# Performance work log

Measured on AMD Instinct MI355X. Metric: run time of the kernel, lower is better.

Reference implementation:

```python
import jax, jax.numpy as jnp
import numpy as np
from functools import partial

B, N, C = 16, 10647, 80   # batch, total anchors (YOLOv3@416), num classes
K = 2048                  # max candidates kept per image before NMS
SCORE_THR = 0.5
IOU_THR = 0.5


def setup_inputs() -> dict:
    key = jax.random.key(0)
    # [B, N, 4+1+C]: xywh (normalized), objectness, class probs
    y_pred = jax.random.uniform(key, (B, N, 5 + C), dtype=jnp.float32)
    return {"y_pred": y_pred}


def _xywh_to_corners(b):
    x, y, w, h = b[..., 0], b[..., 1], b[..., 2], b[..., 3]
    return jnp.stack([x - w / 2, y - h / 2, x + w / 2, y + h / 2], axis=-1)


def _pairwise_iou(boxes):  # boxes [K,4] corners -> [K,K]
    x1, y1, x2, y2 = boxes[:, 0], boxes[:, 1], boxes[:, 2], boxes[:, 3]
    area = jnp.maximum(x2 - x1, 0.0) * jnp.maximum(y2 - y1, 0.0)
    ix1 = jnp.maximum(x1[:, None], x1[None, :])
    iy1 = jnp.maximum(y1[:, None], y1[None, :])
    ix2 = jnp.minimum(x2[:, None], x2[None, :])
    iy2 = jnp.minimum(y2[:, None], y2[None, :])
    inter = jnp.maximum(ix2 - ix1, 0.0) * jnp.maximum(iy2 - iy1, 0.0)
    union = area[:, None] + area[None, :] - inter
    return inter / jnp.maximum(union, 1e-9)


def _greedy_nms_keep(boxes, valid):  # boxes [K,4] sorted by score desc, valid [K] bool
    iou = _pairwise_iou(boxes)
    idxs = jnp.arange(K)

    def body(i, keep):
        suppress = keep[i] & (idxs > i) & (iou[i] > IOU_THR)
        return keep & ~suppress

    return jax.lax.fori_loop(0, K, body, valid)


def reference(y_pred):
    boxes_xywh = y_pred[..., :4]           # [B,N,4]
    obj = y_pred[..., 4]                   # [B,N]
    cls_probs = y_pred[..., 5:]            # [B,N,C]
    scores = obj * jnp.max(cls_probs, axis=-1)  # [B,N]

    # top-K candidates per image (sorted by score desc)
    scores_k, idx = jax.lax.top_k(scores, K)             # [B,K]
    boxes_k = jnp.take_along_axis(boxes_xywh, idx[:, :, None], axis=1)  # [B,K,4]
    corners = _xywh_to_corners(boxes_k)                  # [B,K,4]

    valid = scores_k > SCORE_THR                          # [B,K]
    # NMS keep mask is a non-differentiable selection
    keep = jax.vmap(_greedy_nms_keep)(
        jax.lax.stop_gradient(corners), valid)            # [B,K] bool
    keep_f = keep.astype(scores_k.dtype)

    out_boxes = corners * keep_f[:, :, None]
    out_scores = scores_k * keep_f
    return jnp.concatenate([out_boxes, out_scores[:, :, None]], axis=-1)  # [B,K,5]
```

## Files before the change

kernel.cpp:

```cpp
#include <hip/hip_runtime.h>

#define BATCH 16
#define NROW  10647
#define ROWF  85
#define NCLS  80
#define KTOP  2048
#define MPAD  16384
#define SCORE_THR 0.5f
#define IOU_THR   0.5f

typedef unsigned long long u64;
typedef unsigned int u32;

__device__ __forceinline__ u32 enc_f32(float f) {
    u32 u = __float_as_uint(f);
    return (u & 0x80000000u) ? ~u : (u | 0x80000000u);
}
__device__ __forceinline__ float dec_f32(u32 e) {
    u32 u = (e & 0x80000000u) ? (e & 0x7FFFFFFFu) : ~e;
    return __uint_as_float(u);
}
__device__ __forceinline__ float bcast(float v, int ii) {
    return __uint_as_float(__builtin_amdgcn_readlane(__float_as_uint(v), ii));
}
__device__ __forceinline__ u64 rl64(u64 v, int l) {
    u32 lo = __builtin_amdgcn_readlane((u32)(v & 0xFFFFFFFFull), l);
    u32 hi = __builtin_amdgcn_readlane((u32)(v >> 32), l);
    return ((u64)hi << 32) | (u64)lo;
}
__device__ __forceinline__ void gload_lds16(const void* g, void* lds) {
    __builtin_amdgcn_global_load_lds(
        (const __attribute__((address_space(1))) void*)g,
        (__attribute__((address_space(3))) void*)lds, 16, 0, 0);
}
__device__ __forceinline__ void bar_lds() {
    asm volatile("s_waitcnt lgkmcnt(0)" ::: "memory");
    __builtin_amdgcn_s_barrier();
    __builtin_amdgcn_sched_barrier(0);
}

template<int J>
__device__ __forceinline__ void reg_pass(u64 v[8], int tid, int k) {
    #pragma unroll
    for (int r = 0; r < 8; ++r) {
        if (!(r & J)) {
            bool desc = (((tid * 8 + r) & k) == 0);
            u64 a = v[r], b = v[r | J];
            u64 mx = a > b ? a : b, mn = a > b ? b : a;
            v[r]     = desc ? mx : mn;
            v[r | J] = desc ? mn : mx;
        }
    }
}

__device__ __forceinline__ void shfl_pass(u64 v[8], int tid, int k, int d) {
    const bool upper = (tid & d) == 0;
    const bool desc = (((tid * 8) & k) == 0);
    const bool keepmax = (desc == upper);
    #pragma unroll
    for (int r = 0; r < 8; ++r) {
        u64 pv = __shfl_xor(v[r], d);
        u64 mx = v[r] > pv ? v[r] : pv, mn = v[r] > pv ? pv : v[r];
        v[r] = keepmax ? mx : mn;
    }
}

__device__ __forceinline__ void lds_pass(u64 v[8], int tid, u64* sm, int k, int d) {
    __syncthreads();
    #pragma unroll
    for (int r = 0; r < 8; ++r) sm[r * 256 + tid] = v[r];
    __syncthreads();
    const bool upper = (tid & d) == 0;
    const bool desc = (((tid * 8) & k) == 0);
    const bool keepmax = (desc == upper);
    const int pt = tid ^ d;
    #pragma unroll
    for (int r = 0; r < 8; ++r) {
        u64 pv = sm[r * 256 + pt];
        u64 mx = v[r] > pv ? v[r] : pv, mn = v[r] > pv ? pv : v[r];
        v[r] = keepmax ? mx : mn;
    }
}

__device__ __forceinline__ void sort2048_desc(u64 v[8], int tid, u64* sm) {
    reg_pass<1>(v, tid, 2);
    reg_pass<2>(v, tid, 4); reg_pass<1>(v, tid, 4);
    for (int k = 8; k <= 2048; k <<= 1) {
        for (int j = k >> 1; j >= 8; j >>= 1) {
            int d = j >> 3;
            if (d <= 32) shfl_pass(v, tid, k, d);
            else         lds_pass(v, tid, sm, k, d);
        }
        reg_pass<4>(v, tid, k); reg_pass<2>(v, tid, k); reg_pass<1>(v, tid, k);
    }
}

__device__ __forceinline__ void cleanup2048_desc(u64 v[8], int tid, u64* sm) {
    lds_pass(v, tid, sm, 4096, 128);
    lds_pass(v, tid, sm, 4096, 64);
    for (int d = 32; d >= 1; d >>= 1) shfl_pass(v, tid, 4096, d);
    reg_pass<4>(v, tid, 4096); reg_pass<2>(v, tid, 4096); reg_pass<1>(v, tid, 4096);
}

__global__ void score_kernel(const float* __restrict__ yp, u64* __restrict__ keys) {
    __shared__ float tile[128 * ROWF];
    const int tileIdx = blockIdx.x;
    const int b = blockIdx.y;
    const int tid = threadIdx.x;
    const int batch_lim = NROW * ROWF;
    const int tile_base = tileIdx * 128 * ROWF;

    if (tile_base < batch_lim) {
        const float* src = yp + (long long)b * batch_lim;
        for (int e = tid; e < 128 * ROWF; e += 256) {
            float v = 0.f;
            if (tile_base + e < batch_lim) v = src[tile_base + e];
            tile[e] = v;
        }
    }
    __syncthreads();

    if (tid < 128) {
        int gr = tileIdx * 128 + tid;
        u64 key = 0ULL;
        if (gr < NROW) {
            const float* r = &tile[tid * ROWF];
            float obj = r[4];
            float m = r[5];
            #pragma unroll
            for (int c = 1; c < NCLS; ++c) m = fmaxf(m, r[5 + c]);
            float s = obj * m;
            key = ((u64)enc_f32(s) << 32) | (u64)(0xFFFFFFFFu - (u32)gr);
        }
        keys[(long long)b * MPAD + gr] = key;
    }
}

__global__ void chunk_sort_kernel(u64* __restrict__ keys) {
    __shared__ u64 sm[2048];
    const int b = blockIdx.y, c = blockIdx.x, tid = threadIdx.x;
    u64* base = keys + (long long)b * MPAD + c * 2048;
    u64 v[8];
    #pragma unroll
    for (int r = 0; r < 8; ++r) v[r] = base[tid * 8 + r];
    sort2048_desc(v, tid, sm);
    #pragma unroll
    for (int r = 0; r < 8; ++r) base[tid * 8 + r] = v[r];
}

__global__ void merge_all_kernel(const u64* __restrict__ keysA,
                                 const float* __restrict__ yp,
                                 float* __restrict__ sx1, float* __restrict__ sy1,
                                 float* __restrict__ sx2, float* __restrict__ sy2,
                                 float* __restrict__ sar, float* __restrict__ ssc) {
    __shared__ u64 sm[2048];
    __shared__ u64 buf[3][2048];
    const int b = blockIdx.x, tid = threadIdx.x;
    const u64* a = keysA + (long long)b * MPAD;
    u64 v[8];

    #pragma unroll
    for (int c = 0; c < 3; ++c) {
        const u64* p = a + c * 4096;
        #pragma unroll
        for (int r = 0; r < 8; ++r) {
            int e = tid * 8 + r;
            u64 va = p[e], vb = p[4095 - e];
            v[r] = va > vb ? va : vb;
        }
        cleanup2048_desc(v, tid, sm);
        #pragma unroll
        for (int r = 0; r < 8; ++r) buf[c][tid * 8 + r] = v[r];
    }
    __syncthreads();

    #pragma unroll
    for (int r = 0; r < 8; ++r) {
        int e = tid * 8 + r;
        u64 va = buf[0][e], vb = buf[1][2047 - e];
        v[r] = va > vb ? va : vb;
    }
    cleanup2048_desc(v, tid, sm);

    #pragma unroll
    for (int r = 0; r < 8; ++r) {
        int e = tid * 8 + r;
        u64 vb = buf[2][2047 - e];
        v[r] = v[r] > vb ? v[r] : vb;
    }
    cleanup2048_desc(v, tid, sm);

    #pragma unroll
    for (int r = 0; r < 8; ++r) {
        u64 key = v[r];
        float s = dec_f32((u32)(key >> 32));
        u32 idx = 0xFFFFFFFFu - (u32)(key & 0xFFFFFFFFu);
        const float* rp = yp + (long long)b * NROW * ROWF + (long long)idx * ROWF;
        float x = rp[0], y = rp[1], w = rp[2], h = rp[3];
        float hx = w * 0.5f, hy = h * 0.5f;
        float a1 = x - hx, b1 = y - hy, a2 = x + hx, b2 = y + hy;
        int o = b * KTOP + tid * 8 + r;
        sx1[o] = a1; sy1[o] = b1; sx2[o] = a2; sy2[o] = b2;
        sar[o] = fmaxf(a2 - a1, 0.f) * fmaxf(b2 - b1, 0.f);
        ssc[o] = s;
    }
}

__global__ void mask_kernel(const float* __restrict__ sx1, const float* __restrict__ sy1,
                            const float* __restrict__ sx2, const float* __restrict__ sy2,
                            const float* __restrict__ sar, u64* __restrict__ mask) {
    const int b = blockIdx.y;
    const int t = blockIdx.x * 4 + (threadIdx.x >> 6);
    const int lane = threadIdx.x & 63;

    int rb = (int)((65.0f - sqrtf(4225.0f - 8.0f * (float)t)) * 0.5f);
    while (rb * (65 - rb) / 2 > t) --rb;
    while ((rb + 1) * (64 - rb) / 2 <= t) ++rb;
    const int cb = rb + t - rb * (65 - rb) / 2;

    const int oi = b * KTOP + rb * 64 + lane;
    const int oj = b * KTOP + cb * 64 + lane;
    const float rx1 = sx1[oi], ry1 = sy1[oi], rx2 = sx2[oi], ry2 = sy2[oi], ra = sar[oi];
    const float cx1 = sx1[oj], cy1 = sy1[oj], cx2 = sx2[oj], cy2 = sy2[oj], ca = sar[oj];
    const bool diag = (rb == cb);

    u64 myword = 0ULL;
    for (int ii = 0; ii < 64; ++ii) {
        float ax1 = bcast(rx1, ii), ay1 = bcast(ry1, ii);
        float ax2 = bcast(rx2, ii), ay2 = bcast(ry2, ii);
        float aa  = bcast(ra,  ii);
        float ix1 = fmaxf(ax1, cx1);
        float iy1 = fmaxf(ay1, cy1);
        float ix2 = fminf(ax2, cx2);
        float iy2 = fminf(ay2, cy2);
        float inter = fmaxf(ix2 - ix1, 0.f) * fmaxf(iy2 - iy1, 0.f);
        float uni = aa + ca - inter;
        float iou = inter / fmaxf(uni, 1e-9f);
        bool cond = (iou > IOU_THR) && (!diag || (lane > ii));
        u64 bal = __ballot(cond);
        if (lane == ii) myword = bal;
    }
    mask[(long long)(b * KTOP + rb * 64 + lane) * 32 + cb] = myword;
}

__global__ void nms_out_kernel(const float* __restrict__ sx1, const float* __restrict__ sy1,
                               const float* __restrict__ sx2, const float* __restrict__ sy2,
                               const float* __restrict__ ssc,
                               const u64* __restrict__ mask, float* __restrict__ out) {
    __shared__ u64 slots[4][2048];
    __shared__ u64 pend[8][32];
    __shared__ u64 curs;
    __shared__ u64 sbits64[32];
    __shared__ u64 keepw[32];
    const int b = blockIdx.x;
    const int tid = threadIdx.x;
    const int lane = tid & 63;
    const int wave = tid >> 6;
    const u64* mb = mask + (long long)(b * KTOP) * 32;
    const char* mbc = (const char*)mb;

    auto issue_block = [&](int B) {
        const char* src = mbc + (size_t)B * 16384;
        char* dst = (char*)&slots[B & 3][0];
        #pragma unroll
        for (int i = 0; i < 16; ++i)
            gload_lds16(src + i * 1024 + lane * 16, dst + i * 1024);
    };

    {
        const float* sp = ssc + b * KTOP + tid * 8;
        float4 sa = *(const float4*)(sp);
        float4 sb = *(const float4*)(sp + 4);
        unsigned bits =
            (unsigned)(sa.x > SCORE_THR)       | ((unsigned)(sa.y > SCORE_THR) << 1) |
            ((unsigned)(sa.z > SCORE_THR) << 2) | ((unsigned)(sa.w > SCORE_THR) << 3) |
            ((unsigned)(sb.x > SCORE_THR) << 4) | ((unsigned)(sb.y > SCORE_THR) << 5) |
            ((unsigned)(sb.z > SCORE_THR) << 6) | ((unsigned)(sb.w > SCORE_THR) << 7);
        ((unsigned char*)sbits64)[tid] = (unsigned char)bits;
    }
    if (wave >= 1) issue_block(wave - 1);
    __syncthreads();

    u64 myw = 0ULL;
    if (wave == 0 && lane < 32) myw = sbits64[lane];

    u64 cur = 0ULL;
    #pragma unroll 1
    for (int w = 0; w < 32; ++w) {
        const u64* blk = &slots[w & 3][0];

        if (wave == 0) {
            u64 dia = blk[(size_t)lane * 32 + w];
            u64 cv = __shfl(myw, w);
            cur = ((u64)(u32)__builtin_amdgcn_readfirstlane((u32)(cv >> 32)) << 32)
                | (u64)(u32)__builtin_amdgcn_readfirstlane((u32)cv);
            #pragma unroll
            for (int p = 0; p < 4; ++p) {
                u64 dd[16];
                #pragma unroll
                for (int i = 0; i < 16; ++i) dd[i] = rl64(dia, p * 16 + i);
                #pragma unroll
                for (int i = 0; i < 16; ++i) {
                    u64 m = ((cur >> (p * 16 + i)) & 1ULL) ? dd[i] : 0ULL;
                    cur &= ~m;
                }
            }
            if (lane == 0) curs = cur;
        } else {
            const int rr = wave - 1;
            if ((w % 3) == rr && w + 3 < 32) issue_block(w + 3);
            if (((w + 1) % 3) == rr)
                asm volatile("s_waitcnt vmcnt(0)" ::: "memory");
        }
        bar_lds();

        {
            u64 curv = curs;
            const int col = tid & 31;
            const int rg  = tid >> 5;
            const u64* rp = blk + (size_t)rg * 256 + col;
            u32 bits8 = (u32)(curv >> (rg * 8)) & 0xFFu;
            u64 acc = 0ULL;
            #pragma unroll
            for (int i = 0; i < 8; ++i) {
                u64 t = rp[(size_t)i * 32];
                acc |= ((bits8 >> i) & 1u) ? t : 0ULL;
            }
            pend[rg][col] = acc;
        }
        bar_lds();

        if (wave == 0 && lane < 32) {
            u64 s = ((pend[0][lane] | pend[1][lane]) | (pend[2][lane] | pend[3][lane]))
                  | ((pend[4][lane] | pend[5][lane]) | (pend[6][lane] | pend[7][lane]));
            if (lane == w) myw = cur;
            else if (lane > w) myw &= ~s;
        }
    }

    if (wave == 0 && lane < 32) keepw[lane] = myw;
    __syncthreads();

    for (int t = tid; t < KTOP; t += 256) {
        int o = b * KTOP + t;
        float f = ((keepw[t >> 6] >> (t & 63)) & 1ULL) ? 1.0f : 0.0f;
        float* op = out + (long long)o * 5;
        op[0] = sx1[o] * f;
        op[1] = sy1[o] * f;
        op[2] = sx2[o] * f;
        op[3] = sy2[o] * f;
        op[4] = ssc[o] * f;
    }
}

extern "C" void kernel_launch(void* const* d_in, const int* in_sizes, int n_in,
                              void* d_out, int out_size, void* d_ws, size_t ws_size,
                              hipStream_t stream) {
    const float* yp = (const float*)d_in[0];
    float* out = (float*)d_out;
    char* ws = (char*)d_ws;

    const size_t MASK_BYTES = (size_t)BATCH * KTOP * 32 * sizeof(u64);
    u64* keysA = (u64*)ws;
    u64* mask  = (u64*)ws;
    float* soa = (float*)(ws + MASK_BYTES);
    const int SA = BATCH * KTOP;
    float* sx1 = soa + 0 * SA;
    float* sy1 = soa + 1 * SA;
    float* sx2 = soa + 2 * SA;
    float* sy2 = soa + 3 * SA;
    float* sar = soa + 4 * SA;
    float* ssc = soa + 5 * SA;

    score_kernel<<<dim3(128, BATCH), 256, 0, stream>>>(yp, keysA);
    chunk_sort_kernel<<<dim3(6, BATCH), 256, 0, stream>>>(keysA);
    merge_all_kernel<<<BATCH, 256, 0, stream>>>(keysA, yp, sx1, sy1, sx2, sy2, sar, ssc);
    mask_kernel<<<dim3(132, BATCH), 256, 0, stream>>>(sx1, sy1, sx2, sy2, sar, mask);
    nms_out_kernel<<<BATCH, 256, 0, stream>>>(sx1, sy1, sx2, sy2, ssc, mask, out);
}
```

Baseline: 188.4 us.

## Prefetch NMS diagonal mask words separately and vectorize score tile loads

The mask kernel now also writes each diagonal 64x64 block's words to a small separate buffer. The serial NMS loop reads the next diagonal word from global memory one iteration ahead, instead of loading it from the LDS slot inside the critical chain. It also takes the current keep word with a readlane rather than shuffle plus readfirstlane. The score kernel loads its tile with aligned float4 loads plus scalar head and tail handling, and launches 96 tiles instead of 128, which drops blocks that only wrote padding. The cost is extra global writes and workspace, and the padding keys above 12288 are no longer written.

```diff
diff --git a/kernel.cpp b/kernel.cpp
--- a/kernel.cpp
+++ b/kernel.cpp
@@ -111,11 +111,22 @@
     const int tile_base = tileIdx * 128 * ROWF;
 
     if (tile_base < batch_lim) {
-        const float* src = yp + (long long)b * batch_lim;
-        for (int e = tid; e < 128 * ROWF; e += 256) {
-            float v = 0.f;
-            if (tile_base + e < batch_lim) v = src[tile_base + e];
-            tile[e] = v;
+        const float* src = yp + (long long)b * batch_lim + tile_base;
+        int lim_e = batch_lim - tile_base;
+        if (lim_e > 128 * ROWF) lim_e = 128 * ROWF;
+        const int head = (4 - ((3 * b) & 3)) & 3;
+        if (lim_e >= 8) {
+            const int nv = (lim_e - head) >> 2;
+            for (int e = tid; e < head; e += 256) tile[e] = src[e];
+            const float4* s4 = (const float4*)(src + head);
+            for (int q = tid; q < nv; q += 256) {
+                float4 v = s4[q];
+                int o = head + q * 4;
+                tile[o] = v.x; tile[o + 1] = v.y; tile[o + 2] = v.z; tile[o + 3] = v.w;
+            }
+            for (int e = head + nv * 4 + tid; e < lim_e; e += 256) tile[e] = src[e];
+        } else {
+            for (int e = tid; e < lim_e; e += 256) tile[e] = src[e];
         }
     }
     __syncthreads();
@@ -208,7 +219,8 @@
 
 __global__ void mask_kernel(const float* __restrict__ sx1, const float* __restrict__ sy1,
                             const float* __restrict__ sx2, const float* __restrict__ sy2,
-                            const float* __restrict__ sar, u64* __restrict__ mask) {
+                            const float* __restrict__ sar, u64* __restrict__ mask,
+                            u64* __restrict__ diag) {
     const int b = blockIdx.y;
     const int t = blockIdx.x * 4 + (threadIdx.x >> 6);
     const int lane = threadIdx.x & 63;
@@ -222,7 +234,7 @@
     const int oj = b * KTOP + cb * 64 + lane;
     const float rx1 = sx1[oi], ry1 = sy1[oi], rx2 = sx2[oi], ry2 = sy2[oi], ra = sar[oi];
     const float cx1 = sx1[oj], cy1 = sy1[oj], cx2 = sx2[oj], cy2 = sy2[oj], ca = sar[oj];
-    const bool diag = (rb == cb);
+    const bool dg = (rb == cb);
 
     u64 myword = 0ULL;
     for (int ii = 0; ii < 64; ++ii) {
@@ -236,17 +248,19 @@
         float inter = fmaxf(ix2 - ix1, 0.f) * fmaxf(iy2 - iy1, 0.f);
         float uni = aa + ca - inter;
         float iou = inter / fmaxf(uni, 1e-9f);
-        bool cond = (iou > IOU_THR) && (!diag || (lane > ii));
+        bool cond = (iou > IOU_THR) && (!dg || (lane > ii));
         u64 bal = __ballot(cond);
         if (lane == ii) myword = bal;
     }
     mask[(long long)(b * KTOP + rb * 64 + lane) * 32 + cb] = myword;
+    if (dg) diag[(long long)b * 2048 + rb * 64 + lane] = myword;
 }
 
 __global__ void nms_out_kernel(const float* __restrict__ sx1, const float* __restrict__ sy1,
                                const float* __restrict__ sx2, const float* __restrict__ sy2,
                                const float* __restrict__ ssc,
-                               const u64* __restrict__ mask, float* __restrict__ out) {
+                               const u64* __restrict__ mask,
+                               const u64* __restrict__ diag, float* __restrict__ out) {
     __shared__ u64 slots[4][2048];
     __shared__ u64 pend[8][32];
     __shared__ u64 curs;
@@ -258,6 +272,7 @@
     const int wave = tid >> 6;
     const u64* mb = mask + (long long)(b * KTOP) * 32;
     const char* mbc = (const char*)mb;
+    const u64* dg = diag + (long long)b * 2048;
 
     auto issue_block = [&](int B) {
         const char* src = mbc + (size_t)B * 16384;
@@ -278,22 +293,22 @@
             ((unsigned)(sb.z > SCORE_THR) << 6) | ((unsigned)(sb.w > SCORE_THR) << 7);
         ((unsigned char*)sbits64)[tid] = (unsigned char)bits;
     }
+    u64 dia = 0ULL;
+    if (wave == 0) dia = dg[lane];
     if (wave >= 1) issue_block(wave - 1);
     __syncthreads();
 
     u64 myw = 0ULL;
     if (wave == 0 && lane < 32) myw = sbits64[lane];
 
-    u64 cur = 0ULL;
     #pragma unroll 1
     for (int w = 0; w < 32; ++w) {
         const u64* blk = &slots[w & 3][0];
 
         if (wave == 0) {
-            u64 dia = blk[(size_t)lane * 32 + w];
-            u64 cv = __shfl(myw, w);
-            cur = ((u64)(u32)__builtin_amdgcn_readfirstlane((u32)(cv >> 32)) << 32)
-                | (u64)(u32)__builtin_amdgcn_readfirstlane((u32)cv);
+            u64 dia_next = 0ULL;
+            if (w < 31) dia_next = dg[(w + 1) * 64 + lane];
+            u64 cur = rl64(myw, w);
             #pragma unroll
             for (int p = 0; p < 4; ++p) {
                 u64 dd[16];
@@ -306,6 +321,7 @@
                 }
             }
             if (lane == 0) curs = cur;
+            dia = dia_next;
         } else {
             const int rr = wave - 1;
             if ((w % 3) == rr && w + 3 < 32) issue_block(w + 3);
@@ -331,6 +347,7 @@
         bar_lds();
 
         if (wave == 0 && lane < 32) {
+            u64 cur = curs;
             u64 s = ((pend[0][lane] | pend[1][lane]) | (pend[2][lane] | pend[3][lane]))
                   | ((pend[4][lane] | pend[5][lane]) | (pend[6][lane] | pend[7][lane]));
             if (lane == w) myw = cur;
@@ -361,9 +378,11 @@
     char* ws = (char*)d_ws;
 
     const size_t MASK_BYTES = (size_t)BATCH * KTOP * 32 * sizeof(u64);
+    const size_t SOA_BYTES  = (size_t)6 * BATCH * KTOP * sizeof(float);
     u64* keysA = (u64*)ws;
     u64* mask  = (u64*)ws;
     float* soa = (float*)(ws + MASK_BYTES);
+    u64* diag  = (u64*)(ws + MASK_BYTES + SOA_BYTES);
     const int SA = BATCH * KTOP;
     float* sx1 = soa + 0 * SA;
     float* sy1 = soa + 1 * SA;
@@ -372,9 +391,9 @@
     float* sar = soa + 4 * SA;
     float* ssc = soa + 5 * SA;
 
-    score_kernel<<<dim3(128, BATCH), 256, 0, stream>>>(yp, keysA);
+    score_kernel<<<dim3(96, BATCH), 256, 0, stream>>>(yp, keysA);
     chunk_sort_kernel<<<dim3(6, BATCH), 256, 0, stream>>>(keysA);
     merge_all_kernel<<<BATCH, 256, 0, stream>>>(keysA, yp, sx1, sy1, sx2, sy2, sar, ssc);
-    mask_kernel<<<dim3(132, BATCH), 256, 0, stream>>>(sx1, sy1, sx2, sy2, sar, mask);
-    nms_out_kernel<<<BATCH, 256, 0, stream>>>(sx1, sy1, sx2, sy2, ssc, mask, out);
-}
+    mask_kernel<<<dim3(132, BATCH), 256, 0, stream>>>(sx1, sy1, sx2, sy2, sar, mask, diag);
+    nms_out_kernel<<<BATCH, 256, 0, stream>>>(sx1, sy1, sx2, sy2, ssc, mask, diag, out);
+}
```

Result: faster. 165.8 us (-12.0%).
